# Kernel tuning notes

Measured on AMD Instinct MI355X. Metric: run time of the kernel, lower is better.

Reference implementation:

```python
import jax, jax.numpy as jnp
import numpy as np
from jax import lax

B, T_IN, T_OUT, E, U, V = 32, 128, 128, 512, 512, 9000


def reverse_seq(x, lens):
    # tf.reverse_sequence along time axis 1
    T = x.shape[1]
    t = jnp.arange(T)[None, :]
    idx = jnp.where(t < lens[:, None], lens[:, None] - 1 - t, t)
    return jnp.take_along_axis(x, idx[:, :, None], axis=1)


def run_lstm(x, lens, kernel, bias):
    """TF LSTMCell (gate order i,j,f,o, forget_bias=1.0) with dynamic_rnn
    length semantics: zero outputs and frozen state past seq_len."""
    T = x.shape[1]
    units = bias.shape[0] // 4
    xT = jnp.swapaxes(x, 0, 1)  # [T,B,D]
    c0 = jnp.zeros((x.shape[0], units), x.dtype)
    h0 = jnp.zeros_like(c0)

    def step(carry, xs):
        c, h = carry
        xt, t = xs
        z = jnp.concatenate([xt, h], axis=-1) @ kernel + bias
        i, j, f, o = jnp.split(z, 4, axis=-1)
        c_new = jax.nn.sigmoid(f + 1.0) * c + jax.nn.sigmoid(i) * jnp.tanh(j)
        h_new = jax.nn.sigmoid(o) * jnp.tanh(c_new)
        valid = (t < lens)[:, None]
        c2 = jnp.where(valid, c_new, c)
        h2 = jnp.where(valid, h_new, h)
        out = jnp.where(valid, h_new, 0.0)
        return (c2, h2), out

    (c, h), outs = lax.scan(step, (c0, h0), (xT, jnp.arange(T)))
    return jnp.swapaxes(outs, 0, 1), (c, h)


def setup_inputs() -> dict:
    key = jax.random.key(0)
    ks = jax.random.split(key, 20)
    s = 0.05
    inp = {
        "embed_in": jax.random.normal(ks[0], (B, T_IN, E), jnp.float32),
        "dec_embed": jax.random.normal(ks[1], (B, T_OUT, E), jnp.float32),
        "in_seq_len": jax.random.randint(ks[2], (B,), T_IN // 2, T_IN + 1).astype(jnp.int32),
        # encoder fw/bw LSTM (input E, units U)
        "enc_fw_kernel": jax.random.normal(ks[3], (E + U, 4 * U), jnp.float32) * s,
        "enc_fw_bias": jnp.zeros((4 * U,), jnp.float32),
        "enc_bw_kernel": jax.random.normal(ks[4], (E + U, 4 * U), jnp.float32) * s,
        "enc_bw_bias": jnp.zeros((4 * U,), jnp.float32),
        # decoder layer0 input = concat(embed, attention) -> E+U
        "dec_kernel0": jax.random.normal(ks[5], (E + U + U, 4 * U), jnp.float32) * s,
        "dec_bias0": jnp.zeros((4 * U,), jnp.float32),
        "dec_kernel1": jax.random.normal(ks[6], (U + U, 4 * U), jnp.float32) * s,
        "dec_bias1": jnp.zeros((4 * U,), jnp.float32),
        # normalized Bahdanau attention
        "w_mem": jax.random.normal(ks[7], (2 * U, U), jnp.float32) * s,
        "w_query": jax.random.normal(ks[8], (U, U), jnp.float32) * s,
        "b_attn": jnp.zeros((U,), jnp.float32),
        "v_attn": jax.random.normal(ks[9], (U,), jnp.float32),
        "g_attn": jnp.asarray(np.sqrt(1.0 / U), jnp.float32),
        # attention layer: Linear(concat(cell_out, context)) no bias
        "w_attn_layer": jax.random.normal(ks[10], (U + 2 * U, U), jnp.float32) * s,
        # output projection to vocab
        "w_proj": jax.random.normal(ks[11], (U, V), jnp.float32) * s,
        "b_proj": jnp.zeros((V,), jnp.float32),
    }
    return inp


def reference(embed_in, dec_embed, in_seq_len,
              enc_fw_kernel, enc_fw_bias, enc_bw_kernel, enc_bw_bias,
              dec_kernel0, dec_bias0, dec_kernel1, dec_bias1,
              w_mem, w_query, b_attn, v_attn, g_attn,
              w_attn_layer, w_proj, b_proj):
    lens = in_seq_len
    # ---- bidirectional encoder ----
    fw_out, (c_fw, h_fw) = run_lstm(embed_in, lens, enc_fw_kernel, enc_fw_bias)
    x_rev = reverse_seq(embed_in, lens)
    bw_out_rev, (c_bw, h_bw) = run_lstm(x_rev, lens, enc_bw_kernel, enc_bw_bias)
    bw_out = reverse_seq(bw_out_rev, lens)
    enc_out = jnp.concatenate([fw_out, bw_out], axis=-1)  # [B,Tin,2U]

    # ---- normalized Bahdanau attention precompute ----
    keys = jnp.einsum('btd,du->btu', enc_out, w_mem)  # [B,Tin,U]
    v_norm = g_attn * v_attn / jnp.sqrt(jnp.sum(v_attn * v_attn))
    t_idx = jnp.arange(enc_out.shape[1])[None, :]
    attn_mask = t_idx < lens[:, None]  # [B,Tin]
    neg = jnp.asarray(-1e9, enc_out.dtype)

    # decoder initial state from encoder final states (fw->layer0, bw->layer1)
    a0 = jnp.zeros((embed_in.shape[0], keys.shape[-1]), embed_in.dtype)
    carry0 = (c_fw, h_fw, c_bw, h_bw, a0)

    def lstm_step(xt, c, h, kernel, bias):
        z = jnp.concatenate([xt, h], axis=-1) @ kernel + bias
        i, j, f, o = jnp.split(z, 4, axis=-1)
        c_new = jax.nn.sigmoid(f + 1.0) * c + jax.nn.sigmoid(i) * jnp.tanh(j)
        h_new = jax.nn.sigmoid(o) * jnp.tanh(c_new)
        return c_new, h_new

    def dec_step(carry, x_t):
        c0, h0, c1, h1, attn = carry
        cell_in = jnp.concatenate([x_t, attn], axis=-1)  # AttentionWrapper input
        c0n, h0n = lstm_step(cell_in, c0, h0, dec_kernel0, dec_bias0)
        c1n, h1n = lstm_step(h0n, c1, h1, dec_kernel1, dec_bias1)
        q = h1n @ w_query  # [B,U]
        score = jnp.einsum('btu,u->bt', jnp.tanh(keys + q[:, None, :] + b_attn), v_norm)
        score = jnp.where(attn_mask, score, neg)
        alpha = jax.nn.softmax(score, axis=-1)
        context = jnp.einsum('bt,btd->bd', alpha, enc_out)  # [B,2U]
        attn_new = jnp.concatenate([h1n, context], axis=-1) @ w_attn_layer  # [B,U]
        return (c0n, h0n, c1n, h1n, attn_new), attn_new

    xT = jnp.swapaxes(dec_embed, 0, 1)  # [Tout,B,E]
    _, dec_outs = lax.scan(dec_step, carry0, xT)
    dec_outs = jnp.swapaxes(dec_outs, 0, 1)  # [B,Tout,U]
    logits = dec_outs @ w_proj + b_proj  # [B,Tout,V]
    return logits
```

## Files before the change

### kernel.cpp

```cpp
#include <hip/hip_runtime.h>
#include <stdint.h>

#define NTHR 256
#define NBLKS 512

namespace cfg {
constexpr size_t F_CELLS = 0;
constexpr size_t F_H0    = 524288;
constexpr size_t F_C0    = F_H0 + 16384;
constexpr size_t F_H1    = F_C0 + 16384;
constexpr size_t F_C1    = F_H1 + 16384;
constexpr size_t F_ATTNS = F_C1 + 16384;
constexpr size_t F_VN    = F_ATTNS + 32768;
constexpr size_t F_CTX   = F_VN + 512;
constexpr size_t F_AALL  = F_CTX + 32768;
constexpr size_t F_EOUT  = F_AALL + 2097152;
constexpr size_t F_KEYS  = F_EOUT + 4194304;
constexpr size_t F_TOTAL = F_KEYS + 2097152;
constexpr size_t MEMSET_BYTES = F_VN * 4;
constexpr size_t O_P0 = 0;
constexpr size_t O_P1 = 786432;
}

__device__ __forceinline__ float sigm(float x)   { return 1.0f / (1.0f + __expf(-x)); }
__device__ __forceinline__ float tanhft(float x) { return 1.0f - 2.0f / (1.0f + __expf(2.0f * x)); }

__device__ __forceinline__ float cload(const float* p) {
  return __hip_atomic_load(p, __ATOMIC_RELAXED, __HIP_MEMORY_SCOPE_AGENT);
}
__device__ __forceinline__ void cstore(float* p, float v) {
  __hip_atomic_store(p, v, __ATOMIC_RELAXED, __HIP_MEMORY_SCOPE_AGENT);
}

__device__ __forceinline__ void gbar(unsigned ep, unsigned* arr, unsigned* rel) {
  __syncthreads();
  if (blockIdx.x == 0) {
    if (threadIdx.x == 0)
      __hip_atomic_store(arr, ep, __ATOMIC_RELAXED, __HIP_MEMORY_SCOPE_AGENT);
    int s0 = threadIdx.x, s1 = threadIdx.x + 256;
    while (__hip_atomic_load(arr + s0, __ATOMIC_RELAXED, __HIP_MEMORY_SCOPE_AGENT) < ep)
      __builtin_amdgcn_s_sleep(1);
    while (__hip_atomic_load(arr + s1, __ATOMIC_RELAXED, __HIP_MEMORY_SCOPE_AGENT) < ep)
      __builtin_amdgcn_s_sleep(1);
    __syncthreads();
    __hip_atomic_store(rel + (size_t)s0 * 32, ep, __ATOMIC_RELAXED, __HIP_MEMORY_SCOPE_AGENT);
    __hip_atomic_store(rel + (size_t)s1 * 32, ep, __ATOMIC_RELAXED, __HIP_MEMORY_SCOPE_AGENT);
    __syncthreads();
  } else {
    if (threadIdx.x == 0) {
      __hip_atomic_store(arr + blockIdx.x, ep, __ATOMIC_RELAXED, __HIP_MEMORY_SCOPE_AGENT);
      while (__hip_atomic_load(rel + (size_t)blockIdx.x * 32, __ATOMIC_RELAXED,
                               __HIP_MEMORY_SCOPE_AGENT) < ep)
        __builtin_amdgcn_s_sleep(1);
    }
    __syncthreads();
  }
}

template<int KWIN, typename F>
__device__ __forceinline__ void stage(float* at, F&& f) {
  static_assert((32 * KWIN) % NTHR == 0, "tile must tile NTHR");
  constexpr int PER = (32 * KWIN) / NTHR;
  __syncthreads();
  float v[PER];
#pragma unroll
  for (int r = 0; r < PER; r++) {
    int i = threadIdx.x + NTHR * r;
    v[r] = f(i / KWIN, i % KWIN);
  }
#pragma unroll
  for (int r = 0; r < PER; r++) at[threadIdx.x + NTHR * r] = v[r];
  __syncthreads();
}

template<int KWIN>
__device__ __forceinline__ void gemm_frag(const float* __restrict__ W, int ldw,
                                          int n, bool nok, int kw0,
                                          const float* at, float* acc) {
  const int wave = threadIdx.x >> 6;
  constexpr int KQ = KWIN / 4;
  const int klo = wave * KQ;
  const float* wp = W + (size_t)(kw0 + klo) * (size_t)ldw + n;
  float w[KQ];
#pragma unroll
  for (int j = 0; j < KQ; j++) w[j] = nok ? wp[(size_t)j * ldw] : 0.f;
#pragma unroll
  for (int jj = 0; jj < KQ; jj += 4) {
    const float* ap = at + klo + jj;
#pragma unroll
    for (int m = 0; m < 32; m++) {
      float4 a = *(const float4*)(ap + m * KWIN);
      acc[m] = fmaf(a.x, w[jj + 0], acc[m]);
      acc[m] = fmaf(a.y, w[jj + 1], acc[m]);
      acc[m] = fmaf(a.z, w[jj + 2], acc[m]);
      acc[m] = fmaf(a.w, w[jj + 3], acc[m]);
    }
  }
}

__device__ __forceinline__ void red_write(float* red, const float* acc) {
  const int wave = threadIdx.x >> 6, lane = threadIdx.x & 63;
  __syncthreads();
#pragma unroll
  for (int m = 0; m < 32; m++) red[(wave * 32 + m) * 64 + lane] = acc[m];
  __syncthreads();
}
__device__ __forceinline__ float redsum(const float* red, int m, int c) {
  return red[m * 64 + c] + red[2048 + m * 64 + c] +
         red[4096 + m * 64 + c] + red[6144 + m * 64 + c];
}

__device__ __forceinline__ void epi_cstore(const float* red, float* outp, int ldo, int n0) {
  for (int i = threadIdx.x; i < 2048; i += NTHR) {
    int m = i >> 6, nn = i & 63;
    cstore(outp + (size_t)m * ldo + n0 + nn, redsum(red, m, nn));
  }
}

template<int NKB>
__device__ __forceinline__ void gate_sum4(const float* base, float g4[4]) {
  float v[4][NKB];
#pragma unroll
  for (int g = 0; g < 4; g++) {
    const float* p = base + g * 512;
#pragma unroll
    for (int j = 0; j < NKB; j++) v[g][j] = cload(p + (size_t)j * 65536);
  }
#pragma unroll
  for (int g = 0; g < 4; g++) {
    float s = 0.f;
#pragma unroll
    for (int j = 0; j < NKB; j++) s += v[g][j];
    g4[g] = s;
  }
}

__global__ __launch_bounds__(NTHR, 2) void seq2seq_kernel(
    const float* __restrict__ embed_in, const float* __restrict__ dec_embed,
    const int* __restrict__ lens,
    const float* __restrict__ Wfw, const float* __restrict__ bfw,
    const float* __restrict__ Wbw, const float* __restrict__ bbw,
    const float* __restrict__ Wd0, const float* __restrict__ bd0,
    const float* __restrict__ Wd1, const float* __restrict__ bd1,
    const float* __restrict__ Wmem, const float* __restrict__ Wq,
    const float* __restrict__ battn, const float* __restrict__ vattn,
    const float* __restrict__ gattn, const float* __restrict__ Wal,
    const float* __restrict__ Wproj, const float* __restrict__ bproj,
    float* __restrict__ out, float* ws) {
  __shared__ float smem[12288];
  float* at  = smem;
  float* red = smem + 4096;

  unsigned* arr = (unsigned*)ws;
  unsigned* rel = (unsigned*)ws + 512;
  float* h0     = ws + cfg::F_H0;
  float* c0     = ws + cfg::F_C0;
  float* h1     = ws + cfg::F_H1;
  float* c1     = ws + cfg::F_C1;
  float* attn_s = ws + cfg::F_ATTNS;
  float* vn     = ws + cfg::F_VN;
  float* ctx    = ws + cfg::F_CTX;
  float* aall   = ws + cfg::F_AALL;
  float* eout   = ws + cfg::F_EOUT;
  float* keysp  = ws + cfg::F_KEYS;
  float* p0     = out + cfg::O_P0;
  float* p1     = out + cfg::O_P1;

  const int bid = blockIdx.x, tid = threadIdx.x;
  const int wave = tid >> 6, lane = tid & 63;
  unsigned ep = 1;
#define BAR()  do { gbar(ep, arr, rel); ep++; } while (0)
#define BARSEAL() do { __threadfence(); gbar(ep, arr, rel); ep++; __threadfence(); } while (0)

  if (bid == 0) {
    float s = 0.f;
    for (int u = tid; u < 512; u += NTHR) { float x = vattn[u]; s = fmaf(x, x, s); }
#pragma unroll
    for (int off = 32; off > 0; off >>= 1) s += __shfl_xor(s, off, 64);
    if (lane == 0) at[64 + wave] = s;
    __syncthreads();
    float S = at[64] + at[65] + at[66] + at[67];
    float scale = gattn[0] / sqrtf(S);
    for (int u = tid; u < 512; u += NTHR) vn[u] = vattn[u] * scale;
  }
  BAR();

  for (int t = 0; t < 128; t++) {
    {
      int dir = bid >> 8;
      int r = bid & 255;
      int nb = r & 31, kb = r >> 5;
      const float* W = dir ? Wbw : Wfw;
      const float* hs = dir ? h1 : h0;
      stage<128>(at, [&](int m, int kl) -> float {
        int kk = kb * 128 + kl;
        if (kk < 512) {
          int tt = t;
          if (dir) { int len = lens[m]; tt = (t < len) ? (len - 1 - t) : t; }
          return embed_in[((size_t)m * 128 + tt) * 512 + kk];
        }
        return cload(hs + m * 512 + kk - 512);
      });
      float acc[32];
#pragma unroll
      for (int m = 0; m < 32; m++) acc[m] = 0.f;
      gemm_frag<128>(W, 2048, nb * 64 + lane, true, kb * 128, at, acc);
      red_write(red, acc);
      epi_cstore(red, (dir ? p1 : p0) + (size_t)kb * 65536, 2048, nb * 64);
    }
    BAR();
    if (bid < 128) {
      int dir = bid >> 6;
      int p = (bid & 63) * NTHR + tid;
      int m = p >> 9, u = p & 511;
      const float* parts = dir ? p1 : p0;
      const float* bias  = dir ? bbw : bfw;
      float* hs = dir ? h1 : h0;
      float* cs = dir ? c1 : c0;
      float g4[4];
      gate_sum4<8>(parts + m * 2048 + u, g4);
#pragma unroll
      for (int g = 0; g < 4; g++) g4[g] += bias[g * 512 + u];
      int len = lens[m];
      bool valid = t < len;
      float co = cload(cs + m * 512 + u);
      float cn = sigm(g4[2] + 1.f) * co + sigm(g4[0]) * tanhft(g4[1]);
      float hn = sigm(g4[3]) * tanhft(cn);
      if (valid) { cstore(cs + m * 512 + u, cn); cstore(hs + m * 512 + u, hn); }
      int tpos = dir ? (valid ? (len - 1 - t) : t) : t;
      eout[((size_t)m * 128 + tpos) * 1024 + dir * 512 + u] = valid ? hn : 0.f;
    }
    BAR();
  }

  BARSEAL();

  {
#pragma unroll 1
    for (int task = bid; task < 1024; task += NBLKS) {
      int mt = task >> 3, nb = task & 7;
      int n0 = nb * 64;
      const float* arow = eout + (size_t)mt * 32 * 1024;
      float acc[32];
#pragma unroll
      for (int m = 0; m < 32; m++) acc[m] = 0.f;
      const int n = n0 + lane;
#pragma unroll 1
      for (int c = 0; c < 8; c++) {
        stage<128>(at, [&](int m, int kl) -> float {
          return arow[(size_t)m * 1024 + c * 128 + kl];
        });
        gemm_frag<128>(Wmem, 512, n, true, c * 128, at, acc);
      }
      red_write(red, acc);
      for (int i = tid; i < 2048; i += NTHR) {
        int m = i >> 6, nn = i & 63;
        keysp[(size_t)mt * 32 * 512 + (size_t)m * 512 + n0 + nn] = redsum(red, m, nn);
      }
    }
  }
  BARSEAL();

  for (int t = 0; t < 128; t++) {
    if (bid < 384) {
      int nb = bid & 31, kb = bid >> 5;
      const float* asrc = attn_s + (size_t)((t + 1) & 1) * 16384;
      stage<128>(at, [&](int m, int kl) -> float {
        int kk = kb * 128 + kl;
        if (kk < 512) return dec_embed[((size_t)m * 128 + t) * 512 + kk];
        if (kk < 1024) return cload(asrc + m * 512 + kk - 512);
        return cload(h0 + m * 512 + kk - 1024);
      });
      float acc[32];
#pragma unroll
      for (int m = 0; m < 32; m++) acc[m] = 0.f;
      gemm_frag<128>(Wd0, 2048, nb * 64 + lane, true, kb * 128, at, acc);
      red_write(red, acc);
      epi_cstore(red, p0 + (size_t)kb * 65536, 2048, nb * 64);
    } else if (bid < 392 && t >= 1) {
      const float* asrc = attn_s + (size_t)((t + 1) & 1) * 16384;
      float v[8];
      int j8 = ((bid - 384) * 256 + tid) * 8;
#pragma unroll
      for (int k = 0; k < 8; k++) v[k] = cload(asrc + j8 + k);
#pragma unroll
      for (int k = 0; k < 8; k++) aall[(size_t)(t - 1) * 16384 + j8 + k] = v[k];
    }
    BAR();

    if (bid < 64) {
      int p = bid * NTHR + tid;
      int m = p >> 9, u = p & 511;
      float g4[4];
      gate_sum4<12>(p0 + m * 2048 + u, g4);
#pragma unroll
      for (int g = 0; g < 4; g++) g4[g] += bd0[g * 512 + u];
      float co = cload(c0 + m * 512 + u);
      float cn = sigm(g4[2] + 1.f) * co + sigm(g4[0]) * tanhft(g4[1]);
      float hn = sigm(g4[3]) * tanhft(cn);
      cstore(c0 + m * 512 + u, cn);
      cstore(h0 + m * 512 + u, hn);
    } else if (bid < 72) {
      float* az = attn_s + (size_t)(t & 1) * 16384 + (size_t)(bid - 64) * 2048;
      for (int i = tid; i < 2048; i += NTHR) cstore(az + i, 0.f);
    }
    BAR();

    {
      int nb = bid & 31, kb = bid >> 5;
      stage<64>(at, [&](int m, int kl) -> float {
        int kk = kb * 64 + kl;
        return (kk < 512) ? cload(h0 + m * 512 + kk) : cload(h1 + m * 512 + kk - 512);
      });
      float acc[32];
#pragma unroll
      for (int m = 0; m < 32; m++) acc[m] = 0.f;
      gemm_frag<64>(Wd1, 2048, nb * 64 + lane, true, kb * 64, at, acc);
      red_write(red, acc);
      epi_cstore(red, p1 + (size_t)kb * 65536, 2048, nb * 64);
    }
    BAR();

    if (bid < 32) {
      int b = bid;
      int len = lens[b];
      float* sh_h1v = at;
      float* sh_qb  = at + 512;
      float* sh_vnv = at + 1024;
      float* sh_sc  = at + 1536;
      float* sh_al  = at + 1664;
      float* sh_r   = at + 1792;
      float* redq   = at + 2048;
#pragma unroll 1
      for (int u = tid; u < 512; u += NTHR) {
        float g4[4];
        gate_sum4<16>(p1 + b * 2048 + u, g4);
#pragma unroll
        for (int g = 0; g < 4; g++) g4[g] += bd1[g * 512 + u];
        float co = cload(c1 + b * 512 + u);
        float cn = sigm(g4[2] + 1.f) * co + sigm(g4[0]) * tanhft(g4[1]);
        float hn = sigm(g4[3]) * tanhft(cn);
        cstore(c1 + b * 512 + u, cn);
        cstore(h1 + b * 512 + u, hn);
        sh_h1v[u] = hn;
        sh_vnv[u] = vn[u];
      }
      __syncthreads();
      {
        float4 qa = make_float4(0.f, 0.f, 0.f, 0.f), qb4 = make_float4(0.f, 0.f, 0.f, 0.f);
        const int ua = lane * 4, ub = 256 + lane * 4;
        const float* wqp = Wq + (size_t)(wave * 128) * 512;
#pragma unroll 1
        for (int kk = 0; kk < 128; kk += 8) {
          float4 wa[8], wb[8];
#pragma unroll
          for (int j = 0; j < 8; j++) {
            wa[j] = *(const float4*)(wqp + (size_t)(kk + j) * 512 + ua);
            wb[j] = *(const float4*)(wqp + (size_t)(kk + j) * 512 + ub);
          }
#pragma unroll
          for (int j = 0; j < 8; j++) {
            float h = sh_h1v[wave * 128 + kk + j];
            qa.x = fmaf(h, wa[j].x, qa.x); qa.y = fmaf(h, wa[j].y, qa.y);
            qa.z = fmaf(h, wa[j].z, qa.z); qa.w = fmaf(h, wa[j].w, qa.w);
            qb4.x = fmaf(h, wb[j].x, qb4.x); qb4.y = fmaf(h, wb[j].y, qb4.y);
            qb4.z = fmaf(h, wb[j].z, qb4.z); qb4.w = fmaf(h, wb[j].w, qb4.w);
          }
        }
        *(float4*)(redq + wave * 512 + ua) = qa;
        *(float4*)(redq + wave * 512 + ub) = qb4;
      }
      __syncthreads();
      for (int u = tid; u < 512; u += NTHR)
        sh_qb[u] = redq[u] + redq[512 + u] + redq[1024 + u] + redq[1536 + u] + battn[u];
      __syncthreads();
#pragma unroll 1
      for (int tt = 0; tt < 32; tt += 4) {
        float4 kv[4][2];
#pragma unroll
        for (int j = 0; j < 4; j++) {
          const float* kp = keysp + ((size_t)b * 128 + wave * 32 + tt + j) * 512;
          kv[j][0] = *(const float4*)(kp + lane * 4);
          kv[j][1] = *(const float4*)(kp + lane * 4 + 256);
        }
#pragma unroll
        for (int j = 0; j < 4; j++) {
          int tq = wave * 32 + tt + j;
          float s = 0.f;
#pragma unroll
          for (int hh = 0; hh < 2; hh++) {
            int u = lane * 4 + hh * 256;
            float4 k4 = kv[j][hh];
            s += sh_vnv[u + 0] * tanhft(k4.x + sh_qb[u + 0]);
            s += sh_vnv[u + 1] * tanhft(k4.y + sh_qb[u + 1]);
            s += sh_vnv[u + 2] * tanhft(k4.z + sh_qb[u + 2]);
            s += sh_vnv[u + 3] * tanhft(k4.w + sh_qb[u + 3]);
          }
#pragma unroll
          for (int off = 32; off > 0; off >>= 1) s += __shfl_xor(s, off, 64);
          if (lane == 0) sh_sc[tq] = (tq < len) ? s : -1e30f;
        }
      }
      __syncthreads();
      {
        float v = (tid < 128) ? sh_sc[tid] : -1e30f;
        float mx = v;
#pragma unroll
        for (int off = 32; off > 0; off >>= 1) mx = fmaxf(mx, __shfl_xor(mx, off, 64));
        if (lane == 0) sh_r[wave] = mx;
        __syncthreads();
        mx = fmaxf(fmaxf(sh_r[0], sh_r[1]), fmaxf(sh_r[2], sh_r[3]));
        float e = (tid < 128 && tid < len) ? __expf(v - mx) : 0.f;
        float sum = e;
#pragma unroll
        for (int off = 32; off > 0; off >>= 1) sum += __shfl_xor(sum, off, 64);
        if (lane == 0) sh_r[8 + wave] = sum;
        __syncthreads();
        float inv = 1.f / (sh_r[8] + sh_r[9] + sh_r[10] + sh_r[11]);
        if (tid < 128) sh_al[tid] = e * inv;
      }
      __syncthreads();
      {
        int d = tid * 4;
        float4 acc = make_float4(0.f, 0.f, 0.f, 0.f);
        const float* ep2 = eout + (size_t)b * 128 * 1024 + d;
#pragma unroll 1
        for (int tq0 = 0; tq0 < 128; tq0 += 8) {
          float4 e4[8];
#pragma unroll
          for (int j = 0; j < 8; j++)
            e4[j] = *(const float4*)(ep2 + (size_t)(tq0 + j) * 1024);
#pragma unroll
          for (int j = 0; j < 8; j++) {
            float a = sh_al[tq0 + j];
            acc.x = fmaf(a, e4[j].x, acc.x); acc.y = fmaf(a, e4[j].y, acc.y);
            acc.z = fmaf(a, e4[j].z, acc.z); acc.w = fmaf(a, e4[j].w, acc.w);
          }
        }
        cstore(ctx + b * 1024 + d + 0, acc.x);
        cstore(ctx + b * 1024 + d + 1, acc.y);
        cstore(ctx + b * 1024 + d + 2, acc.z);
        cstore(ctx + b * 1024 + d + 3, acc.w);
      }
    }
    BAR();

    if (bid < 128) {
      int nb = bid & 7, kb = bid >> 3;
      stage<96>(at, [&](int m, int kl) -> float {
        int kk = kb * 96 + kl;
        return (kk < 512) ? cload(h1 + m * 512 + kk) : cload(ctx + m * 1024 + kk - 512);
      });
      float acc[32];
#pragma unroll
      for (int m = 0; m < 32; m++) acc[m] = 0.f;
      gemm_frag<96>(Wal, 512, nb * 64 + lane, true, kb * 96, at, acc);
      red_write(red, acc);
      float* adst = attn_s + (size_t)(t & 1) * 16384;
      for (int i = tid; i < 2048; i += NTHR) {
        int m = i >> 6, nn = i & 63;
        atomicAdd(adst + (size_t)m * 512 + nb * 64 + nn, redsum(red, m, nn));
      }
    }
    BAR();
  }

  if (bid >= 384 && bid < 392) {
    const float* asrc = attn_s + (size_t)1 * 16384;
    float v[8];
    int j8 = ((bid - 384) * 256 + tid) * 8;
#pragma unroll
    for (int k = 0; k < 8; k++) v[k] = cload(asrc + j8 + k);
#pragma unroll
    for (int k = 0; k < 8; k++) aall[(size_t)127 * 16384 + j8 + k] = v[k];
  }
  BARSEAL();

#pragma unroll 1
  for (int task = bid; task < 564; task += NBLKS) {
    int nb = task >> 2, tq = task & 3;
    int n0 = nb * 64;
    const int col = n0 + lane;
    const bool ok = col < 9000;
#pragma unroll 1
    for (int t = tq * 32; t < tq * 32 + 32; t++) {
      const float* asrc = aall + (size_t)t * 16384;
      float acc[32];
#pragma unroll
      for (int m = 0; m < 32; m++) acc[m] = 0.f;
#pragma unroll 1
      for (int c = 0; c < 4; c++) {
        stage<128>(at, [&](int m, int kl) -> float {
          return asrc[(size_t)m * 512 + c * 128 + kl];
        });
        gemm_frag<128>(Wproj, 9000, col, ok, c * 128, at, acc);
      }
      red_write(red, acc);
      for (int i = tid; i < 2048; i += NTHR) {
        int m = i >> 6, nn = i & 63;
        int nc = n0 + nn;
        if (nc < 9000)
          out[((size_t)m * 128 + t) * 9000 + nc] = redsum(red, m, nn) + bproj[nc];
      }
    }
  }
#undef BAR
#undef BARSEAL
}

extern "C" void kernel_launch(void* const* d_in, const int* in_sizes, int n_in,
                              void* d_out, int out_size, void* d_ws, size_t ws_size,
                              hipStream_t stream) {
  (void)in_sizes; (void)n_in; (void)out_size; (void)ws_size;
  hipMemsetAsync(d_ws, 0, cfg::MEMSET_BYTES, stream);
  hipLaunchKernelGGL(seq2seq_kernel, dim3(NBLKS), dim3(NTHR), 0, stream,
                     (const float*)d_in[0],
                     (const float*)d_in[1],
                     (const int*)d_in[2],
                     (const float*)d_in[3],
                     (const float*)d_in[4],
                     (const float*)d_in[5],
                     (const float*)d_in[6],
                     (const float*)d_in[7],
                     (const float*)d_in[8],
                     (const float*)d_in[9],
                     (const float*)d_in[10],
                     (const float*)d_in[11],
                     (const float*)d_in[12],
                     (const float*)d_in[13],
                     (const float*)d_in[14],
                     (const float*)d_in[15],
                     (const float*)d_in[16],
                     (const float*)d_in[17],
                     (const float*)d_in[18],
                     (float*)d_out, (float*)d_ws);
}
```

Baseline: 19.02 ms.

## Widen K-split windows in recurrent GEMMs to halve blocks and partial sums

The encoder, decoder layer-0, layer-1 and attention-layer GEMMs now give each block a K window twice as wide (256 or 192 instead of 128/64/96). This halves the number of participating blocks and the partial-sum slices that the gate kernels reduce. gemm_frag gains a sub-chunk loop so the per-thread weight register array stays bounded, and shared memory grows to hold the larger activation tile. The aim is to cut partial-sum traffic and reduction work on the latency-bound recurrent steps. The cost is fewer blocks doing more serial work each, with larger shared-memory staging per block.

```diff
diff --git a/kernel.cpp b/kernel.cpp
--- a/kernel.cpp
+++ b/kernel.cpp
@@ -19,7 +19,7 @@
 constexpr size_t F_TOTAL = F_KEYS + 2097152;
 constexpr size_t MEMSET_BYTES = F_VN * 4;
 constexpr size_t O_P0 = 0;
-constexpr size_t O_P1 = 786432;
+constexpr size_t O_P1 = 393216;
 }
 
 __device__ __forceinline__ float sigm(float x)   { return 1.0f / (1.0f + __expf(-x)); }
@@ -73,27 +73,31 @@
   __syncthreads();
 }
 
-template<int KWIN>
+template<int KWIN, int KQSUB>
 __device__ __forceinline__ void gemm_frag(const float* __restrict__ W, int ldw,
                                           int n, bool nok, int kw0,
                                           const float* at, float* acc) {
   const int wave = threadIdx.x >> 6;
   constexpr int KQ = KWIN / 4;
+  static_assert(KQ % KQSUB == 0 && KQSUB % 4 == 0, "bad KQSUB");
   const int klo = wave * KQ;
-  const float* wp = W + (size_t)(kw0 + klo) * (size_t)ldw + n;
-  float w[KQ];
-#pragma unroll
-  for (int j = 0; j < KQ; j++) w[j] = nok ? wp[(size_t)j * ldw] : 0.f;
-#pragma unroll
-  for (int jj = 0; jj < KQ; jj += 4) {
-    const float* ap = at + klo + jj;
-#pragma unroll
-    for (int m = 0; m < 32; m++) {
-      float4 a = *(const float4*)(ap + m * KWIN);
-      acc[m] = fmaf(a.x, w[jj + 0], acc[m]);
-      acc[m] = fmaf(a.y, w[jj + 1], acc[m]);
-      acc[m] = fmaf(a.z, w[jj + 2], acc[m]);
-      acc[m] = fmaf(a.w, w[jj + 3], acc[m]);
+#pragma unroll 1
+  for (int kk0 = 0; kk0 < KQ; kk0 += KQSUB) {
+    const float* wp = W + (size_t)(kw0 + klo + kk0) * (size_t)ldw + n;
+    float w[KQSUB];
+#pragma unroll
+    for (int j = 0; j < KQSUB; j++) w[j] = nok ? wp[(size_t)j * ldw] : 0.f;
+#pragma unroll
+    for (int jj = 0; jj < KQSUB; jj += 4) {
+      const float* ap = at + klo + kk0 + jj;
+#pragma unroll
+      for (int m = 0; m < 32; m++) {
+        float4 a = *(const float4*)(ap + m * KWIN);
+        acc[m] = fmaf(a.x, w[jj + 0], acc[m]);
+        acc[m] = fmaf(a.y, w[jj + 1], acc[m]);
+        acc[m] = fmaf(a.z, w[jj + 2], acc[m]);
+        acc[m] = fmaf(a.w, w[jj + 3], acc[m]);
+      }
     }
   }
 }
@@ -147,9 +151,9 @@
     const float* __restrict__ gattn, const float* __restrict__ Wal,
     const float* __restrict__ Wproj, const float* __restrict__ bproj,
     float* __restrict__ out, float* ws) {
-  __shared__ float smem[12288];
+  __shared__ float smem[16384];
   float* at  = smem;
-  float* red = smem + 4096;
+  float* red = smem + 8192;
 
   unsigned* arr = (unsigned*)ws;
   unsigned* rel = (unsigned*)ws + 512;
@@ -186,14 +190,14 @@
   BAR();
 
   for (int t = 0; t < 128; t++) {
-    {
-      int dir = bid >> 8;
-      int r = bid & 255;
+    if (bid < 256) {
+      int dir = bid >> 7;
+      int r = bid & 127;
       int nb = r & 31, kb = r >> 5;
       const float* W = dir ? Wbw : Wfw;
       const float* hs = dir ? h1 : h0;
-      stage<128>(at, [&](int m, int kl) -> float {
-        int kk = kb * 128 + kl;
+      stage<256>(at, [&](int m, int kl) -> float {
+        int kk = kb * 256 + kl;
         if (kk < 512) {
           int tt = t;
           if (dir) { int len = lens[m]; tt = (t < len) ? (len - 1 - t) : t; }
@@ -204,7 +208,7 @@
       float acc[32];
 #pragma unroll
       for (int m = 0; m < 32; m++) acc[m] = 0.f;
-      gemm_frag<128>(W, 2048, nb * 64 + lane, true, kb * 128, at, acc);
+      gemm_frag<256, 32>(W, 2048, nb * 64 + lane, true, kb * 256, at, acc);
       red_write(red, acc);
       epi_cstore(red, (dir ? p1 : p0) + (size_t)kb * 65536, 2048, nb * 64);
     }
@@ -218,7 +222,7 @@
       float* hs = dir ? h1 : h0;
       float* cs = dir ? c1 : c0;
       float g4[4];
-      gate_sum4<8>(parts + m * 2048 + u, g4);
+      gate_sum4<4>(parts + m * 2048 + u, g4);
 #pragma unroll
       for (int g = 0; g < 4; g++) g4[g] += bias[g * 512 + u];
       int len = lens[m];
@@ -250,7 +254,7 @@
         stage<128>(at, [&](int m, int kl) -> float {
           return arow[(size_t)m * 1024 + c * 128 + kl];
         });
-        gemm_frag<128>(Wmem, 512, n, true, c * 128, at, acc);
+        gemm_frag<128, 32>(Wmem, 512, n, true, c * 128, at, acc);
       }
       red_write(red, acc);
       for (int i = tid; i < 2048; i += NTHR) {
@@ -262,11 +266,11 @@
   BARSEAL();
 
   for (int t = 0; t < 128; t++) {
-    if (bid < 384) {
+    if (bid < 192) {
       int nb = bid & 31, kb = bid >> 5;
       const float* asrc = attn_s + (size_t)((t + 1) & 1) * 16384;
-      stage<128>(at, [&](int m, int kl) -> float {
-        int kk = kb * 128 + kl;
+      stage<256>(at, [&](int m, int kl) -> float {
+        int kk = kb * 256 + kl;
         if (kk < 512) return dec_embed[((size_t)m * 128 + t) * 512 + kk];
         if (kk < 1024) return cload(asrc + m * 512 + kk - 512);
         return cload(h0 + m * 512 + kk - 1024);
@@ -274,10 +278,10 @@
       float acc[32];
 #pragma unroll
       for (int m = 0; m < 32; m++) acc[m] = 0.f;
-      gemm_frag<128>(Wd0, 2048, nb * 64 + lane, true, kb * 128, at, acc);
+      gemm_frag<256, 32>(Wd0, 2048, nb * 64 + lane, true, kb * 256, at, acc);
       red_write(red, acc);
       epi_cstore(red, p0 + (size_t)kb * 65536, 2048, nb * 64);
-    } else if (bid < 392 && t >= 1) {
+    } else if (bid >= 384 && bid < 392 && t >= 1) {
       const float* asrc = attn_s + (size_t)((t + 1) & 1) * 16384;
       float v[8];
       int j8 = ((bid - 384) * 256 + tid) * 8;
@@ -292,7 +296,7 @@
       int p = bid * NTHR + tid;
       int m = p >> 9, u = p & 511;
       float g4[4];
-      gate_sum4<12>(p0 + m * 2048 + u, g4);
+      gate_sum4<6>(p0 + m * 2048 + u, g4);
 #pragma unroll
       for (int g = 0; g < 4; g++) g4[g] += bd0[g * 512 + u];
       float co = cload(c0 + m * 512 + u);
@@ -306,16 +310,16 @@
     }
     BAR();
 
-    {
+    if (bid < 128) {
       int nb = bid & 31, kb = bid >> 5;
-      stage<64>(at, [&](int m, int kl) -> float {
-        int kk = kb * 64 + kl;
+      stage<256>(at, [&](int m, int kl) -> float {
+        int kk = kb * 256 + kl;
         return (kk < 512) ? cload(h0 + m * 512 + kk) : cload(h1 + m * 512 + kk - 512);
       });
       float acc[32];
 #pragma unroll
       for (int m = 0; m < 32; m++) acc[m] = 0.f;
-      gemm_frag<64>(Wd1, 2048, nb * 64 + lane, true, kb * 64, at, acc);
+      gemm_frag<256, 32>(Wd1, 2048, nb * 64 + lane, true, kb * 256, at, acc);
       red_write(red, acc);
       epi_cstore(red, p1 + (size_t)kb * 65536, 2048, nb * 64);
     }
@@ -334,7 +338,7 @@
 #pragma unroll 1
       for (int u = tid; u < 512; u += NTHR) {
         float g4[4];
-        gate_sum4<16>(p1 + b * 2048 + u, g4);
+        gate_sum4<4>(p1 + b * 2048 + u, g4);
 #pragma unroll
         for (int g = 0; g < 4; g++) g4[g] += bd1[g * 512 + u];
         float co = cload(c1 + b * 512 + u);
@@ -445,16 +449,16 @@
     }
     BAR();
 
-    if (bid < 128) {
+    if (bid < 64) {
       int nb = bid & 7, kb = bid >> 3;
-      stage<96>(at, [&](int m, int kl) -> float {
-        int kk = kb * 96 + kl;
+      stage<192>(at, [&](int m, int kl) -> float {
+        int kk = kb * 192 + kl;
         return (kk < 512) ? cload(h1 + m * 512 + kk) : cload(ctx + m * 1024 + kk - 512);
       });
       float acc[32];
 #pragma unroll
       for (int m = 0; m < 32; m++) acc[m] = 0.f;
-      gemm_frag<96>(Wal, 512, nb * 64 + lane, true, kb * 96, at, acc);
+      gemm_frag<192, 24>(Wal, 512, nb * 64 + lane, true, kb * 192, at, acc);
       red_write(red, acc);
       float* adst = attn_s + (size_t)(t & 1) * 16384;
       for (int i = tid; i < 2048; i += NTHR) {
@@ -493,7 +497,7 @@
         stage<128>(at, [&](int m, int kl) -> float {
           return asrc[(size_t)m * 512 + c * 128 + kl];
         });
-        gemm_frag<128>(Wproj, 9000, col, ok, c * 128, at, acc);
+        gemm_frag<128, 32>(Wproj, 9000, col, ok, c * 128, at, acc);
       }
       red_write(red, acc);
       for (int i = tid; i < 2048; i += NTHR) {
```

Result: slower. 26.35 ms (+38.6%).

## Halve persistent grid and compute two column tiles per block

Applied to the files above, without the earlier changes.

The persistent kernel now runs 256 blocks instead of 512, at one block per CU. Each block computes two 64-column output tiles of every recurrent GEMM (encoder, decoder layer 0 and 1, attention layer) from the same LDS-staged activation tile, using a new two-accumulator GEMM fragment that walks K in sub-chunks. The global barrier now spins on one flag per thread instead of two. Fewer blocks should make each grid barrier cheaper and reuse the staged activations across two weight columns. The cost is twice the serial work and register pressure per block, halved occupancy, and an extra pass in the output-projection task loop.

```diff
diff --git a/kernel.cpp b/kernel.cpp
--- a/kernel.cpp
+++ b/kernel.cpp
@@ -2,7 +2,7 @@
 #include <stdint.h>
 
 #define NTHR 256
-#define NBLKS 512
+#define NBLKS 256
 
 namespace cfg {
 constexpr size_t F_CELLS = 0;
@@ -37,14 +37,10 @@
   if (blockIdx.x == 0) {
     if (threadIdx.x == 0)
       __hip_atomic_store(arr, ep, __ATOMIC_RELAXED, __HIP_MEMORY_SCOPE_AGENT);
-    int s0 = threadIdx.x, s1 = threadIdx.x + 256;
-    while (__hip_atomic_load(arr + s0, __ATOMIC_RELAXED, __HIP_MEMORY_SCOPE_AGENT) < ep)
-      __builtin_amdgcn_s_sleep(1);
-    while (__hip_atomic_load(arr + s1, __ATOMIC_RELAXED, __HIP_MEMORY_SCOPE_AGENT) < ep)
+    while (__hip_atomic_load(arr + threadIdx.x, __ATOMIC_RELAXED, __HIP_MEMORY_SCOPE_AGENT) < ep)
       __builtin_amdgcn_s_sleep(1);
     __syncthreads();
-    __hip_atomic_store(rel + (size_t)s0 * 32, ep, __ATOMIC_RELAXED, __HIP_MEMORY_SCOPE_AGENT);
-    __hip_atomic_store(rel + (size_t)s1 * 32, ep, __ATOMIC_RELAXED, __HIP_MEMORY_SCOPE_AGENT);
+    __hip_atomic_store(rel + (size_t)threadIdx.x * 32, ep, __ATOMIC_RELAXED, __HIP_MEMORY_SCOPE_AGENT);
     __syncthreads();
   } else {
     if (threadIdx.x == 0) {
@@ -98,6 +94,42 @@
   }
 }
 
+template<int KWIN, int KQSUB>
+__device__ __forceinline__ void gemm_frag2(const float* __restrict__ W, int ldw,
+                                           int n1, int n2, int kw0,
+                                           const float* at, float* accA, float* accB) {
+  const int wave = threadIdx.x >> 6;
+  constexpr int KQ = KWIN / 4;
+  static_assert(KQ % KQSUB == 0 && KQSUB % 4 == 0, "bad KQSUB");
+  const int klo = wave * KQ;
+#pragma unroll 1
+  for (int kk0 = 0; kk0 < KQ; kk0 += KQSUB) {
+    const float* wpA = W + (size_t)(kw0 + klo + kk0) * (size_t)ldw + n1;
+    const float* wpB = W + (size_t)(kw0 + klo + kk0) * (size_t)ldw + n2;
+    float wA[KQSUB], wB[KQSUB];
+#pragma unroll
+    for (int j = 0; j < KQSUB; j++) wA[j] = wpA[(size_t)j * ldw];
+#pragma unroll
+    for (int j = 0; j < KQSUB; j++) wB[j] = wpB[(size_t)j * ldw];
+#pragma unroll
+    for (int jj = 0; jj < KQSUB; jj += 4) {
+      const float* ap = at + klo + kk0 + jj;
+#pragma unroll
+      for (int m = 0; m < 32; m++) {
+        float4 a = *(const float4*)(ap + m * KWIN);
+        accA[m] = fmaf(a.x, wA[jj + 0], accA[m]);
+        accA[m] = fmaf(a.y, wA[jj + 1], accA[m]);
+        accA[m] = fmaf(a.z, wA[jj + 2], accA[m]);
+        accA[m] = fmaf(a.w, wA[jj + 3], accA[m]);
+        accB[m] = fmaf(a.x, wB[jj + 0], accB[m]);
+        accB[m] = fmaf(a.y, wB[jj + 1], accB[m]);
+        accB[m] = fmaf(a.z, wB[jj + 2], accB[m]);
+        accB[m] = fmaf(a.w, wB[jj + 3], accB[m]);
+      }
+    }
+  }
+}
+
 __device__ __forceinline__ void red_write(float* red, const float* acc) {
   const int wave = threadIdx.x >> 6, lane = threadIdx.x & 63;
   __syncthreads();
@@ -135,7 +167,7 @@
   }
 }
 
-__global__ __launch_bounds__(NTHR, 2) void seq2seq_kernel(
+__global__ __launch_bounds__(NTHR, 1) void seq2seq_kernel(
     const float* __restrict__ embed_in, const float* __restrict__ dec_embed,
     const int* __restrict__ lens,
     const float* __restrict__ Wfw, const float* __restrict__ bfw,
@@ -187,9 +219,9 @@
 
   for (int t = 0; t < 128; t++) {
     {
-      int dir = bid >> 8;
-      int r = bid & 255;
-      int nb = r & 31, kb = r >> 5;
+      int dir = bid >> 7;
+      int r = bid & 127;
+      int kb = r >> 4, nbp = r & 15;
       const float* W = dir ? Wbw : Wfw;
       const float* hs = dir ? h1 : h0;
       stage<128>(at, [&](int m, int kl) -> float {
@@ -201,12 +233,16 @@
         }
         return cload(hs + m * 512 + kk - 512);
       });
-      float acc[32];
-#pragma unroll
-      for (int m = 0; m < 32; m++) acc[m] = 0.f;
-      gemm_frag<128>(W, 2048, nb * 64 + lane, true, kb * 128, at, acc);
-      red_write(red, acc);
-      epi_cstore(red, (dir ? p1 : p0) + (size_t)kb * 65536, 2048, nb * 64);
+      float accA[32], accB[32];
+#pragma unroll
+      for (int m = 0; m < 32; m++) { accA[m] = 0.f; accB[m] = 0.f; }
+      gemm_frag2<128, 16>(W, 2048, nbp * 64 + lane, (nbp + 16) * 64 + lane,
+                          kb * 128, at, accA, accB);
+      float* dst = (dir ? p1 : p0) + (size_t)kb * 65536;
+      red_write(red, accA);
+      epi_cstore(red, dst, 2048, nbp * 64);
+      red_write(red, accB);
+      epi_cstore(red, dst, 2048, (nbp + 16) * 64);
     }
     BAR();
     if (bid < 128) {
@@ -262,8 +298,8 @@
   BARSEAL();
 
   for (int t = 0; t < 128; t++) {
-    if (bid < 384) {
-      int nb = bid & 31, kb = bid >> 5;
+    if (bid < 192) {
+      int kb = bid >> 4, nbp = bid & 15;
       const float* asrc = attn_s + (size_t)((t + 1) & 1) * 16384;
       stage<128>(at, [&](int m, int kl) -> float {
         int kk = kb * 128 + kl;
@@ -271,16 +307,20 @@
         if (kk < 1024) return cload(asrc + m * 512 + kk - 512);
         return cload(h0 + m * 512 + kk - 1024);
       });
-      float acc[32];
-#pragma unroll
-      for (int m = 0; m < 32; m++) acc[m] = 0.f;
-      gemm_frag<128>(Wd0, 2048, nb * 64 + lane, true, kb * 128, at, acc);
-      red_write(red, acc);
-      epi_cstore(red, p0 + (size_t)kb * 65536, 2048, nb * 64);
-    } else if (bid < 392 && t >= 1) {
+      float accA[32], accB[32];
+#pragma unroll
+      for (int m = 0; m < 32; m++) { accA[m] = 0.f; accB[m] = 0.f; }
+      gemm_frag2<128, 16>(Wd0, 2048, nbp * 64 + lane, (nbp + 16) * 64 + lane,
+                          kb * 128, at, accA, accB);
+      float* dst = p0 + (size_t)kb * 65536;
+      red_write(red, accA);
+      epi_cstore(red, dst, 2048, nbp * 64);
+      red_write(red, accB);
+      epi_cstore(red, dst, 2048, (nbp + 16) * 64);
+    } else if (bid < 200 && t >= 1) {
       const float* asrc = attn_s + (size_t)((t + 1) & 1) * 16384;
       float v[8];
-      int j8 = ((bid - 384) * 256 + tid) * 8;
+      int j8 = ((bid - 192) * 256 + tid) * 8;
 #pragma unroll
       for (int k = 0; k < 8; k++) v[k] = cload(asrc + j8 + k);
 #pragma unroll
@@ -307,17 +347,21 @@
     BAR();
 
     {
-      int nb = bid & 31, kb = bid >> 5;
+      int kb = bid >> 4, nbp = bid & 15;
       stage<64>(at, [&](int m, int kl) -> float {
         int kk = kb * 64 + kl;
         return (kk < 512) ? cload(h0 + m * 512 + kk) : cload(h1 + m * 512 + kk - 512);
       });
-      float acc[32];
-#pragma unroll
-      for (int m = 0; m < 32; m++) acc[m] = 0.f;
-      gemm_frag<64>(Wd1, 2048, nb * 64 + lane, true, kb * 64, at, acc);
-      red_write(red, acc);
-      epi_cstore(red, p1 + (size_t)kb * 65536, 2048, nb * 64);
+      float accA[32], accB[32];
+#pragma unroll
+      for (int m = 0; m < 32; m++) { accA[m] = 0.f; accB[m] = 0.f; }
+      gemm_frag2<64, 16>(Wd1, 2048, nbp * 64 + lane, (nbp + 16) * 64 + lane,
+                         kb * 64, at, accA, accB);
+      float* dst = p1 + (size_t)kb * 65536;
+      red_write(red, accA);
+      epi_cstore(red, dst, 2048, nbp * 64);
+      red_write(red, accB);
+      epi_cstore(red, dst, 2048, (nbp + 16) * 64);
     }
     BAR();
 
@@ -445,30 +489,36 @@
     }
     BAR();
 
-    if (bid < 128) {
-      int nb = bid & 7, kb = bid >> 3;
+    if (bid < 64) {
+      int kb = bid >> 2, nbp = bid & 3;
       stage<96>(at, [&](int m, int kl) -> float {
         int kk = kb * 96 + kl;
         return (kk < 512) ? cload(h1 + m * 512 + kk) : cload(ctx + m * 1024 + kk - 512);
       });
-      float acc[32];
-#pragma unroll
-      for (int m = 0; m < 32; m++) acc[m] = 0.f;
-      gemm_frag<96>(Wal, 512, nb * 64 + lane, true, kb * 96, at, acc);
-      red_write(red, acc);
+      float accA[32], accB[32];
+#pragma unroll
+      for (int m = 0; m < 32; m++) { accA[m] = 0.f; accB[m] = 0.f; }
+      gemm_frag2<96, 24>(Wal, 512, nbp * 64 + lane, (nbp + 4) * 64 + lane,
+                         kb * 96, at, accA, accB);
       float* adst = attn_s + (size_t)(t & 1) * 16384;
+      red_write(red, accA);
       for (int i = tid; i < 2048; i += NTHR) {
         int m = i >> 6, nn = i & 63;
-        atomicAdd(adst + (size_t)m * 512 + nb * 64 + nn, redsum(red, m, nn));
-      }
-    }
-    BAR();
-  }
-
-  if (bid >= 384 && bid < 392) {
+        atomicAdd(adst + (size_t)m * 512 + nbp * 64 + nn, redsum(red, m, nn));
+      }
+      red_write(red, accB);
+      for (int i = tid; i < 2048; i += NTHR) {
+        int m = i >> 6, nn = i & 63;
+        atomicAdd(adst + (size_t)m * 512 + (nbp + 4) * 64 + nn, redsum(red, m, nn));
+      }
+    }
+    BAR();
+  }
+
+  if (bid >= 192 && bid < 200) {
     const float* asrc = attn_s + (size_t)1 * 16384;
     float v[8];
-    int j8 = ((bid - 384) * 256 + tid) * 8;
+    int j8 = ((bid - 192) * 256 + tid) * 8;
 #pragma unroll
     for (int k = 0; k < 8; k++) v[k] = cload(asrc + j8 + k);
 #pragma unroll
```

Result: slower. 36.64 ms (+92.6%).

## Split decoder attention across 8 blocks per batch row using unnormalized softmax atomics

Applied to the files above, without the earlier changes.

The attention step for each batch row moves from one block to eight, each handling 16 encoder timesteps. Each block computes exp(score) without subtracting the max and atomically adds its partial context and its partial exp-sum into global buffers. Normalization is deferred to the following attention-layer GEMM staging. The c1 state is double-buffered, so redundant blocks can read the old state while sub-block 0 writes the new one. This removes the serial 32-block bottleneck in the per-step attention. In exchange it adds atomics, redundant recomputation of the LSTM cell and query projection in all eight blocks, zeroing work, and a risk of overflow because the max subtraction is gone.

```diff
diff --git a/kernel.cpp b/kernel.cpp
--- a/kernel.cpp
+++ b/kernel.cpp
@@ -6,17 +6,18 @@
 
 namespace cfg {
 constexpr size_t F_CELLS = 0;
-constexpr size_t F_H0    = 524288;
-constexpr size_t F_C0    = F_H0 + 16384;
-constexpr size_t F_H1    = F_C0 + 16384;
-constexpr size_t F_C1    = F_H1 + 16384;
-constexpr size_t F_ATTNS = F_C1 + 16384;
-constexpr size_t F_VN    = F_ATTNS + 32768;
-constexpr size_t F_CTX   = F_VN + 512;
-constexpr size_t F_AALL  = F_CTX + 32768;
-constexpr size_t F_EOUT  = F_AALL + 2097152;
-constexpr size_t F_KEYS  = F_EOUT + 4194304;
-constexpr size_t F_TOTAL = F_KEYS + 2097152;
+constexpr size_t F_H0    = 32768;
+constexpr size_t F_C0    = 49152;
+constexpr size_t F_H1    = 65536;
+constexpr size_t F_C1    = 81920;
+constexpr size_t F_ATTNS = 114688;
+constexpr size_t F_VN    = 147456;
+constexpr size_t F_ESUM  = 147968;
+constexpr size_t F_CTXR  = 148480;
+constexpr size_t F_AALL  = 181248;
+constexpr size_t F_EOUT  = 2278400;
+constexpr size_t F_KEYS  = 6472704;
+constexpr size_t F_TOTAL = 8569856;
 constexpr size_t MEMSET_BYTES = F_VN * 4;
 constexpr size_t O_P0 = 0;
 constexpr size_t O_P1 = 786432;
@@ -159,7 +160,8 @@
   float* c1     = ws + cfg::F_C1;
   float* attn_s = ws + cfg::F_ATTNS;
   float* vn     = ws + cfg::F_VN;
-  float* ctx    = ws + cfg::F_CTX;
+  float* esum   = ws + cfg::F_ESUM;
+  float* ctxr   = ws + cfg::F_CTXR;
   float* aall   = ws + cfg::F_AALL;
   float* eout   = ws + cfg::F_EOUT;
   float* keysp  = ws + cfg::F_KEYS;
@@ -216,7 +218,7 @@
       const float* parts = dir ? p1 : p0;
       const float* bias  = dir ? bbw : bfw;
       float* hs = dir ? h1 : h0;
-      float* cs = dir ? c1 : c0;
+      float* cs = dir ? (c1 + 16384) : c0;
       float g4[4];
       gate_sum4<8>(parts + m * 2048 + u, g4);
 #pragma unroll
@@ -303,6 +305,10 @@
     } else if (bid < 72) {
       float* az = attn_s + (size_t)(t & 1) * 16384 + (size_t)(bid - 64) * 2048;
       for (int i = tid; i < 2048; i += NTHR) cstore(az + i, 0.f);
+    } else if (bid < 80) {
+      float* cz = ctxr + (size_t)(bid - 72) * 4096;
+      for (int i = tid; i < 4096; i += NTHR) cstore(cz + i, 0.f);
+      if (bid == 72 && tid < 32) cstore(esum + tid, 0.f);
     }
     BAR();
 
@@ -321,27 +327,29 @@
     }
     BAR();
 
-    if (bid < 32) {
-      int b = bid;
-      int len = lens[b];
+    if (bid < 256) {
+      const int b = bid >> 3, sub = bid & 7;
+      const int len = lens[b];
       float* sh_h1v = at;
       float* sh_qb  = at + 512;
       float* sh_vnv = at + 1024;
-      float* sh_sc  = at + 1536;
-      float* sh_al  = at + 1664;
-      float* sh_r   = at + 1792;
+      float* sh_e   = at + 1536;
       float* redq   = at + 2048;
+      const float* c1r = c1 + (size_t)((t + 1) & 1) * 16384;
+      float* c1w = c1 + (size_t)(t & 1) * 16384;
 #pragma unroll 1
       for (int u = tid; u < 512; u += NTHR) {
         float g4[4];
         gate_sum4<16>(p1 + b * 2048 + u, g4);
 #pragma unroll
         for (int g = 0; g < 4; g++) g4[g] += bd1[g * 512 + u];
-        float co = cload(c1 + b * 512 + u);
+        float co = cload(c1r + b * 512 + u);
         float cn = sigm(g4[2] + 1.f) * co + sigm(g4[0]) * tanhft(g4[1]);
         float hn = sigm(g4[3]) * tanhft(cn);
-        cstore(c1 + b * 512 + u, cn);
-        cstore(h1 + b * 512 + u, hn);
+        if (sub == 0) {
+          cstore(c1w + b * 512 + u, cn);
+          cstore(h1 + b * 512 + u, hn);
+        }
         sh_h1v[u] = hn;
         sh_vnv[u] = vn[u];
       }
@@ -374,18 +382,17 @@
       for (int u = tid; u < 512; u += NTHR)
         sh_qb[u] = redq[u] + redq[512 + u] + redq[1024 + u] + redq[1536 + u] + battn[u];
       __syncthreads();
-#pragma unroll 1
-      for (int tt = 0; tt < 32; tt += 4) {
+      {
         float4 kv[4][2];
 #pragma unroll
         for (int j = 0; j < 4; j++) {
-          const float* kp = keysp + ((size_t)b * 128 + wave * 32 + tt + j) * 512;
+          const float* kp = keysp + ((size_t)b * 128 + sub * 16 + wave * 4 + j) * 512;
           kv[j][0] = *(const float4*)(kp + lane * 4);
           kv[j][1] = *(const float4*)(kp + lane * 4 + 256);
         }
 #pragma unroll
         for (int j = 0; j < 4; j++) {
-          int tq = wave * 32 + tt + j;
+          int tq = sub * 16 + wave * 4 + j;
           float s = 0.f;
 #pragma unroll
           for (int hh = 0; hh < 2; hh++) {
@@ -398,49 +405,35 @@
           }
 #pragma unroll
           for (int off = 32; off > 0; off >>= 1) s += __shfl_xor(s, off, 64);
-          if (lane == 0) sh_sc[tq] = (tq < len) ? s : -1e30f;
+          if (lane == 0) sh_e[wave * 4 + j] = (tq < len) ? __expf(s) : 0.f;
         }
       }
       __syncthreads();
-      {
-        float v = (tid < 128) ? sh_sc[tid] : -1e30f;
-        float mx = v;
-#pragma unroll
-        for (int off = 32; off > 0; off >>= 1) mx = fmaxf(mx, __shfl_xor(mx, off, 64));
-        if (lane == 0) sh_r[wave] = mx;
-        __syncthreads();
-        mx = fmaxf(fmaxf(sh_r[0], sh_r[1]), fmaxf(sh_r[2], sh_r[3]));
-        float e = (tid < 128 && tid < len) ? __expf(v - mx) : 0.f;
-        float sum = e;
-#pragma unroll
-        for (int off = 32; off > 0; off >>= 1) sum += __shfl_xor(sum, off, 64);
-        if (lane == 0) sh_r[8 + wave] = sum;
-        __syncthreads();
-        float inv = 1.f / (sh_r[8] + sh_r[9] + sh_r[10] + sh_r[11]);
-        if (tid < 128) sh_al[tid] = e * inv;
-      }
-      __syncthreads();
+      if (tid == 0) {
+        float es = 0.f;
+#pragma unroll
+        for (int i = 0; i < 16; i++) es += sh_e[i];
+        atomicAdd(esum + b, es);
+      }
       {
         int d = tid * 4;
+        const float* ep2 = eout + ((size_t)b * 128 + sub * 16) * 1024 + d;
+        float4 e4[16];
+#pragma unroll
+        for (int j = 0; j < 16; j++)
+          e4[j] = *(const float4*)(ep2 + (size_t)j * 1024);
         float4 acc = make_float4(0.f, 0.f, 0.f, 0.f);
-        const float* ep2 = eout + (size_t)b * 128 * 1024 + d;
-#pragma unroll 1
-        for (int tq0 = 0; tq0 < 128; tq0 += 8) {
-          float4 e4[8];
-#pragma unroll
-          for (int j = 0; j < 8; j++)
-            e4[j] = *(const float4*)(ep2 + (size_t)(tq0 + j) * 1024);
-#pragma unroll
-          for (int j = 0; j < 8; j++) {
-            float a = sh_al[tq0 + j];
-            acc.x = fmaf(a, e4[j].x, acc.x); acc.y = fmaf(a, e4[j].y, acc.y);
-            acc.z = fmaf(a, e4[j].z, acc.z); acc.w = fmaf(a, e4[j].w, acc.w);
-          }
+#pragma unroll
+        for (int j = 0; j < 16; j++) {
+          float a = sh_e[j];
+          acc.x = fmaf(a, e4[j].x, acc.x); acc.y = fmaf(a, e4[j].y, acc.y);
+          acc.z = fmaf(a, e4[j].z, acc.z); acc.w = fmaf(a, e4[j].w, acc.w);
         }
-        cstore(ctx + b * 1024 + d + 0, acc.x);
-        cstore(ctx + b * 1024 + d + 1, acc.y);
-        cstore(ctx + b * 1024 + d + 2, acc.z);
-        cstore(ctx + b * 1024 + d + 3, acc.w);
+        float* cp = ctxr + (size_t)b * 1024 + d;
+        atomicAdd(cp + 0, acc.x);
+        atomicAdd(cp + 1, acc.y);
+        atomicAdd(cp + 2, acc.z);
+        atomicAdd(cp + 3, acc.w);
       }
     }
     BAR();
@@ -449,7 +442,9 @@
       int nb = bid & 7, kb = bid >> 3;
       stage<96>(at, [&](int m, int kl) -> float {
         int kk = kb * 96 + kl;
-        return (kk < 512) ? cload(h1 + m * 512 + kk) : cload(ctx + m * 1024 + kk - 512);
+        if (kk < 512) return cload(h1 + m * 512 + kk);
+        float inv = 1.0f / cload(esum + m);
+        return cload(ctxr + (size_t)m * 1024 + kk - 512) * inv;
       });
       float acc[32];
 #pragma unroll
```

New measurement: 18.39 ms. 1.03x faster.
